# Kernel tuning notes

Hardware: AMD Instinct MI355X
Metric: run time of the kernel (lower is better)

The kernel has to match this reference:

```python
import jax, jax.numpy as jnp
import numpy as np
import math

N, S, C, K, V = 32, 4096, 1, 512, 128
TARGET_SCALE = 0.06  # normalize_scale == embedding_scale when normalize=True


def setup_inputs() -> dict:
    key = jax.random.key(0)
    k1, k2 = jax.random.split(key)
    x0 = jax.random.normal(k1, (N, S, C, V), dtype=jnp.float32)
    emb = jax.random.normal(k2, (C, K, V), dtype=jnp.float32) * TARGET_SCALE
    # after_update(): renormalize each code vector to norm = embedding_scale*sqrt(V)
    tn = TARGET_SCALE * math.sqrt(V)
    emb = emb * (tn / jnp.linalg.norm(emb, axis=2, keepdims=True))
    return {"x0": x0, "embedding0": emb}


def _vq_forward(x0, embedding0):
    tn = TARGET_SCALE * math.sqrt(V)
    # normalize inputs and codebook to the same norm (normalize=True path)
    x = tn * x0 / jnp.linalg.norm(x0, axis=3, keepdims=True)              # (N,S,C,V)
    emb = tn * embedding0 / jnp.linalg.norm(embedding0, axis=2, keepdims=True)  # (C,K,V)

    xf = x.reshape(N * S, C, V)
    x2 = jnp.sum(xf * xf, axis=2)                     # (NS, C)
    e2 = jnp.sum(emb * emb, axis=2)                   # (C, K)
    dots = jnp.einsum('ncv,ckv->nck', xf, emb)        # (NS, C, K)
    d2 = x2[:, :, None] + e2[None, :, :] - 2.0 * dots
    index = jnp.argmin(d2, axis=2)                    # (NS, C) int

    # entropy of code usage: histc over n_classes, normalized by len(index)=NS
    hist = jnp.zeros((K,), jnp.float32).at[index.reshape(-1)].add(1.0)
    prob = hist / float(N * S)
    entropy = -jnp.sum(jnp.where(hist > 0, prob * jnp.log(jnp.where(hist > 0, prob, 1.0)), 0.0))

    # gather selected code vectors per channel
    output = emb[jnp.arange(C)[None, :], index]       # (NS, C, V)
    output = output.reshape(x.shape)                  # (N,S,C,V)

    sg = jax.lax.stop_gradient
    out0 = sg(output - x) + x                                              # straight-through
    out1 = jnp.sum((sg(x) - output) ** 2, axis=3)                          # codebook loss (N,S,C)
    out2 = jnp.sum((x - sg(output)) ** 2, axis=3) + jnp.sum((x - x0) ** 2, axis=3)  # commitment + norm penalty
    return out0, out1, out2, entropy


def reference(x0, embedding0):
    return _vq_forward(x0, embedding0)
```

## Files before the change

kernel.cpp:

```cpp
#include <hip/hip_runtime.h>
#include <math.h>

#define VDIM   128
#define KCODES 512
#define NROWS  (32 * 4096)
#define TILE_ROWS 512
#define NBLK (NROWS / TILE_ROWS)
#define TN 0.67882250993908565f

typedef __attribute__((ext_vector_type(8))) short bf16x8;
typedef __attribute__((ext_vector_type(4))) float f32x4;

__device__ __forceinline__ unsigned short f2bf(float f) {
    unsigned u = __float_as_uint(f);
    unsigned r = u + 0x7FFFu + ((u >> 16) & 1u);
    return (unsigned short)(r >> 16);
}

__device__ __forceinline__ bf16x8 pack8(f32x4 a, f32x4 b) {
    bf16x8 v;
    v[0] = (short)f2bf(a[0]); v[1] = (short)f2bf(a[1]);
    v[2] = (short)f2bf(a[2]); v[3] = (short)f2bf(a[3]);
    v[4] = (short)f2bf(b[0]); v[5] = (short)f2bf(b[1]);
    v[6] = (short)f2bf(b[2]); v[7] = (short)f2bf(b[3]);
    return v;
}

__global__ __launch_bounds__(1024, 1) void vq_fused(
        const float* __restrict__ x0,
        const float* __restrict__ emb0,
        unsigned short* __restrict__ hist_part,
        float* __restrict__ out0,
        float* __restrict__ out1,
        float* __restrict__ out2) {
    __shared__ uint4 sB[8192];
    __shared__ float sscale[KCODES];
    __shared__ int   shist[KCODES];

    int t = threadIdx.x;
    int w = t >> 6;
    int l = t & 63;
    int n15 = l & 15;
    int q = l >> 4;

    int rowbase = blockIdx.x * TILE_ROWS + (w << 5);
    f32x4 ax[2][4][2];
    #pragma unroll
    for (int s = 0; s < 2; ++s) {
        const float* xrow = x0 + (size_t)(rowbase + (s << 4) + n15) * VDIM + (q << 3);
        #pragma unroll
        for (int kc = 0; kc < 4; ++kc) {
            const f32x4* xp = (const f32x4*)(xrow + (kc << 5));
            ax[s][kc][0] = xp[0];
            ax[s][kc][1] = xp[1];
        }
    }

    if (t < KCODES) shist[t] = 0;

    #pragma unroll 4
    for (int i = 0; i < 32; ++i) {
        int k = (w << 5) + i;
        const float* row = emb0 + (size_t)k * VDIM;
        float a = row[l];
        float b = row[l + 64];
        float ss = a * a + b * b;
        #pragma unroll
        for (int off = 32; off; off >>= 1) ss += __shfl_xor(ss, off);
        if (l == 0) sscale[k] = TN / sqrtf(ss);
    }
    __syncthreads();

    #pragma unroll
    for (int i = 0; i < 8; ++i) {
        int g = (i << 10) + t;
        int k = ((g >> 8) << 4) | (g & 15);
        int d0 = ((g >> 4) & 15) << 3;
        float s = sscale[k];
        const f32x4* ep = (const f32x4*)(emb0 + (size_t)k * VDIM + d0);
        f32x4 a = ep[0], b = ep[1];
        f32x4 as, bs;
        as[0] = a[0] * s; as[1] = a[1] * s; as[2] = a[2] * s; as[3] = a[3] * s;
        bs[0] = b[0] * s; bs[1] = b[1] * s; bs[2] = b[2] * s; bs[3] = b[3] * s;
        ((bf16x8*)sB)[g] = pack8(as, bs);
    }

    bf16x8 afr[2][4];
    float nsq[2];
    #pragma unroll
    for (int s = 0; s < 2; ++s) {
        float p0 = 0.f, p1 = 0.f;
        #pragma unroll
        for (int kc = 0; kc < 4; ++kc) {
            f32x4 a = ax[s][kc][0], b = ax[s][kc][1];
            p0 = fmaf(a[0], a[0], p0); p1 = fmaf(a[1], a[1], p1);
            p0 = fmaf(a[2], a[2], p0); p1 = fmaf(a[3], a[3], p1);
            p0 = fmaf(b[0], b[0], p0); p1 = fmaf(b[1], b[1], p1);
            p0 = fmaf(b[2], b[2], p0); p1 = fmaf(b[3], b[3], p1);
            afr[s][kc] = pack8(a, b);
        }
        nsq[s] = p0 + p1;
        nsq[s] += __shfl_xor(nsq[s], 16, 64);
        nsq[s] += __shfl_xor(nsq[s], 32, 64);
    }

    float best[2][4];
    int   bidx[2][4];
    #pragma unroll
    for (int s = 0; s < 2; ++s)
        #pragma unroll
        for (int r = 0; r < 4; ++r) { best[s][r] = -3.4e38f; bidx[s][r] = 0; }

    const f32x4 zero4 = {0.f, 0.f, 0.f, 0.f};

    __syncthreads();

    #pragma unroll 2
    for (int cn = 0; cn < 32; ++cn) {
        const bf16x8* bls = ((const bf16x8*)sB) + (cn << 8) + l;
        bf16x8 b0 = bls[0], b1 = bls[64], b2 = bls[128], b3 = bls[192];
        int nbase = (cn << 4) + n15;
        #pragma unroll
        for (int s = 0; s < 2; ++s) {
            f32x4 acc = __builtin_amdgcn_mfma_f32_16x16x32_bf16(afr[s][0], b0, zero4, 0, 0, 0);
            acc = __builtin_amdgcn_mfma_f32_16x16x32_bf16(afr[s][1], b1, acc, 0, 0, 0);
            acc = __builtin_amdgcn_mfma_f32_16x16x32_bf16(afr[s][2], b2, acc, 0, 0, 0);
            acc = __builtin_amdgcn_mfma_f32_16x16x32_bf16(afr[s][3], b3, acc, 0, 0, 0);
            #pragma unroll
            for (int r = 0; r < 4; ++r) {
                float d = acc[r];
                if (d > best[s][r]) { best[s][r] = d; bidx[s][r] = nbase; }
            }
        }
    }

    #pragma unroll
    for (int m = 1; m <= 8; m <<= 1) {
        #pragma unroll
        for (int s = 0; s < 2; ++s)
            #pragma unroll
            for (int r = 0; r < 4; ++r) {
                float ov = __shfl_xor(best[s][r], m, 64);
                int   oi = __shfl_xor(bidx[s][r], m, 64);
                if (ov > best[s][r] || (ov == best[s][r] && oi < bidx[s][r])) {
                    best[s][r] = ov; bidx[s][r] = oi;
                }
            }
    }

    size_t wrow = (size_t)rowbase;
    #pragma unroll
    for (int p = 0; p < 16; ++p) {
        const int a0 = 2 * p, a1 = 2 * p + 1;
        int biLo = __shfl(bidx[a0 >> 4][a0 & 3], ((a0 >> 2) & 3) << 4, 64);
        int biHi = __shfl(bidx[a1 >> 4][a1 & 3], ((a1 >> 2) & 3) << 4, 64);
        int bi = (l >= 32) ? biHi : biLo;
        float s = sscale[bi];
        int v4 = l & 31;
        size_t grow = wrow + (p << 1) + (l >> 5);
        f32x4 e = *((const f32x4*)(emb0 + (size_t)bi * VDIM) + v4);
        f32x4 o;
        o[0] = e[0] * s; o[1] = e[1] * s; o[2] = e[2] * s; o[3] = e[3] * s;
        __builtin_nontemporal_store(o, (f32x4*)(out0 + grow * (size_t)VDIM) + v4);
    }

    #pragma unroll
    for (int s = 0; s < 2; ++s)
        #pragma unroll
        for (int r = 0; r < 4; ++r) {
            int src = (l & 12) << 2;
            float dv = __shfl(best[s][r], src, 64);
            int   bv = __shfl(bidx[s][r], src, 64);
            float nn = __shfl(nsq[s], l & 15, 64);
            bool act = (l < 32) && ((l >> 4) == s) && ((l & 3) == r);
            if (act) {
                size_t row = wrow + l;
                float sc = TN / sqrtf(nn);
                float o1 = 2.f * TN * TN - 2.f * sc * dv;
                __builtin_nontemporal_store(o1, &out1[row]);
                float sm = sc - 1.f;
                __builtin_nontemporal_store(o1 + sm * sm * nn, &out2[row]);
                atomicAdd(&shist[bv], 1);
            }
        }

    __syncthreads();

    if (t < KCODES)
        hist_part[((size_t)blockIdx.x << 9) + t] = (unsigned short)shist[t];
}

__global__ __launch_bounds__(1024) void entropy_k(
        const unsigned short* __restrict__ hp,
        float* __restrict__ out) {
    __shared__ int   s2[1024];
    __shared__ float red[8];
    int t = threadIdx.x;
    int c = t & 511;
    int half = t >> 9;
    int sum = 0;
    #pragma unroll 8
    for (int b = half * 128; b < half * 128 + 128; ++b)
        sum += hp[(b << 9) + c];
    s2[t] = sum;
    __syncthreads();
    if (t < 512) {
        float h = (float)(s2[t] + s2[t + 512]);
        float p = h / (float)NROWS;
        float term = (h > 0.f) ? p * logf(p) : 0.f;
        #pragma unroll
        for (int off = 32; off; off >>= 1) term += __shfl_xor(term, off);
        if ((t & 63) == 0) red[t >> 6] = term;
    }
    __syncthreads();
    if (t == 0) {
        float ssum = 0.f;
        #pragma unroll
        for (int i = 0; i < 8; i++) ssum += red[i];
        out[0] = -ssum;
    }
}

extern "C" void kernel_launch(void* const* d_in, const int* in_sizes, int n_in,
                              void* d_out, int out_size, void* d_ws, size_t ws_size,
                              hipStream_t stream) {
    const float* x0   = (const float*)d_in[0];
    const float* emb0 = (const float*)d_in[1];

    unsigned short* hist_part = (unsigned short*)d_ws;

    float* out  = (float*)d_out;
    float* out0 = out;
    float* out1 = out0 + (size_t)NROWS * VDIM;
    float* out2 = out1 + NROWS;
    float* oent = out2 + NROWS;

    vq_fused<<<NBLK, 1024, 0, stream>>>(x0, emb0, hist_part, out0, out1, out2);
    entropy_k<<<1, 1024, 0, stream>>>(hist_part, oent);
}
```

Baseline: 158.9 us.

## Halve block size, give each wave 64 rows, and stage index via LDS

Blocks drop from 1024 to 512 threads, and each wave now processes 64 rows (four 16-row MFMA groups) instead of 32. This reuses each codebook B-fragment read from LDS across twice as many rows, and launch bounds now allow two blocks per CU. The second half of the x loads is issued after the codebook norm pass so its latency is hidden, with sched_barriers to keep that ordering. The epilogue writes best indices to shared memory and reads them back instead of using shuffle broadcasts. The cost is higher register pressure from 16 accumulator/argmax slots per lane and larger per-block LDS, which could limit occupancy.

```diff
diff --git a/kernel.cpp b/kernel.cpp
--- a/kernel.cpp
+++ b/kernel.cpp
@@ -26,7 +26,7 @@
     return v;
 }
 
-__global__ __launch_bounds__(1024, 1) void vq_fused(
+__global__ __launch_bounds__(512, 2) void vq_fused(
         const float* __restrict__ x0,
         const float* __restrict__ emb0,
         unsigned short* __restrict__ hist_part,
@@ -36,6 +36,7 @@
     __shared__ uint4 sB[8192];
     __shared__ float sscale[KCODES];
     __shared__ int   shist[KCODES];
+    __shared__ int   sbesti[TILE_ROWS];
 
     int t = threadIdx.x;
     int w = t >> 6;
@@ -43,24 +44,26 @@
     int n15 = l & 15;
     int q = l >> 4;
 
-    int rowbase = blockIdx.x * TILE_ROWS + (w << 5);
-    f32x4 ax[2][4][2];
+    int rowbase = blockIdx.x * TILE_ROWS + (w << 6);
+
+    f32x4 ax01[2][4][2];
     #pragma unroll
     for (int s = 0; s < 2; ++s) {
         const float* xrow = x0 + (size_t)(rowbase + (s << 4) + n15) * VDIM + (q << 3);
         #pragma unroll
         for (int kc = 0; kc < 4; ++kc) {
             const f32x4* xp = (const f32x4*)(xrow + (kc << 5));
-            ax[s][kc][0] = xp[0];
-            ax[s][kc][1] = xp[1];
-        }
-    }
+            ax01[s][kc][0] = xp[0];
+            ax01[s][kc][1] = xp[1];
+        }
+    }
+    __builtin_amdgcn_sched_barrier(0);
 
     if (t < KCODES) shist[t] = 0;
 
     #pragma unroll 4
-    for (int i = 0; i < 32; ++i) {
-        int k = (w << 5) + i;
+    for (int i = 0; i < 64; ++i) {
+        int k = (w << 6) + i;
         const float* row = emb0 + (size_t)k * VDIM;
         float a = row[l];
         float b = row[l + 64];
@@ -69,11 +72,25 @@
         for (int off = 32; off; off >>= 1) ss += __shfl_xor(ss, off);
         if (l == 0) sscale[k] = TN / sqrtf(ss);
     }
-    __syncthreads();
-
-    #pragma unroll
-    for (int i = 0; i < 8; ++i) {
-        int g = (i << 10) + t;
+
+    f32x4 ax23[2][4][2];
+    #pragma unroll
+    for (int s = 0; s < 2; ++s) {
+        const float* xrow = x0 + (size_t)(rowbase + ((s + 2) << 4) + n15) * VDIM + (q << 3);
+        #pragma unroll
+        for (int kc = 0; kc < 4; ++kc) {
+            const f32x4* xp = (const f32x4*)(xrow + (kc << 5));
+            ax23[s][kc][0] = xp[0];
+            ax23[s][kc][1] = xp[1];
+        }
+    }
+    __builtin_amdgcn_sched_barrier(0);
+
+    __syncthreads();
+
+    #pragma unroll
+    for (int i = 0; i < 16; ++i) {
+        int g = (i << 9) + t;
         int k = ((g >> 8) << 4) | (g & 15);
         int d0 = ((g >> 4) & 15) << 3;
         float s = sscale[k];
@@ -85,14 +102,14 @@
         ((bf16x8*)sB)[g] = pack8(as, bs);
     }
 
-    bf16x8 afr[2][4];
-    float nsq[2];
+    bf16x8 afr[4][4];
+    float nsq[4];
     #pragma unroll
     for (int s = 0; s < 2; ++s) {
         float p0 = 0.f, p1 = 0.f;
         #pragma unroll
         for (int kc = 0; kc < 4; ++kc) {
-            f32x4 a = ax[s][kc][0], b = ax[s][kc][1];
+            f32x4 a = ax01[s][kc][0], b = ax01[s][kc][1];
             p0 = fmaf(a[0], a[0], p0); p1 = fmaf(a[1], a[1], p1);
             p0 = fmaf(a[2], a[2], p0); p1 = fmaf(a[3], a[3], p1);
             p0 = fmaf(b[0], b[0], p0); p1 = fmaf(b[1], b[1], p1);
@@ -104,16 +121,33 @@
         nsq[s] += __shfl_xor(nsq[s], 32, 64);
     }
 
-    float best[2][4];
-    int   bidx[2][4];
-    #pragma unroll
-    for (int s = 0; s < 2; ++s)
+    __syncthreads();
+
+    #pragma unroll
+    for (int s = 0; s < 2; ++s) {
+        float p0 = 0.f, p1 = 0.f;
+        #pragma unroll
+        for (int kc = 0; kc < 4; ++kc) {
+            f32x4 a = ax23[s][kc][0], b = ax23[s][kc][1];
+            p0 = fmaf(a[0], a[0], p0); p1 = fmaf(a[1], a[1], p1);
+            p0 = fmaf(a[2], a[2], p0); p1 = fmaf(a[3], a[3], p1);
+            p0 = fmaf(b[0], b[0], p0); p1 = fmaf(b[1], b[1], p1);
+            p0 = fmaf(b[2], b[2], p0); p1 = fmaf(b[3], b[3], p1);
+            afr[s + 2][kc] = pack8(a, b);
+        }
+        nsq[s + 2] = p0 + p1;
+        nsq[s + 2] += __shfl_xor(nsq[s + 2], 16, 64);
+        nsq[s + 2] += __shfl_xor(nsq[s + 2], 32, 64);
+    }
+
+    float best[4][4];
+    int   bidx[4][4];
+    #pragma unroll
+    for (int s = 0; s < 4; ++s)
         #pragma unroll
         for (int r = 0; r < 4; ++r) { best[s][r] = -3.4e38f; bidx[s][r] = 0; }
 
     const f32x4 zero4 = {0.f, 0.f, 0.f, 0.f};
-
-    __syncthreads();
 
     #pragma unroll 2
     for (int cn = 0; cn < 32; ++cn) {
@@ -121,7 +155,7 @@
         bf16x8 b0 = bls[0], b1 = bls[64], b2 = bls[128], b3 = bls[192];
         int nbase = (cn << 4) + n15;
         #pragma unroll
-        for (int s = 0; s < 2; ++s) {
+        for (int s = 0; s < 4; ++s) {
             f32x4 acc = __builtin_amdgcn_mfma_f32_16x16x32_bf16(afr[s][0], b0, zero4, 0, 0, 0);
             acc = __builtin_amdgcn_mfma_f32_16x16x32_bf16(afr[s][1], b1, acc, 0, 0, 0);
             acc = __builtin_amdgcn_mfma_f32_16x16x32_bf16(afr[s][2], b2, acc, 0, 0, 0);
@@ -137,7 +171,7 @@
     #pragma unroll
     for (int m = 1; m <= 8; m <<= 1) {
         #pragma unroll
-        for (int s = 0; s < 2; ++s)
+        for (int s = 0; s < 4; ++s)
             #pragma unroll
             for (int r = 0; r < 4; ++r) {
                 float ov = __shfl_xor(best[s][r], m, 64);
@@ -148,41 +182,38 @@
             }
     }
 
-    size_t wrow = (size_t)rowbase;
-    #pragma unroll
-    for (int p = 0; p < 16; ++p) {
-        const int a0 = 2 * p, a1 = 2 * p + 1;
-        int biLo = __shfl(bidx[a0 >> 4][a0 & 3], ((a0 >> 2) & 3) << 4, 64);
-        int biHi = __shfl(bidx[a1 >> 4][a1 & 3], ((a1 >> 2) & 3) << 4, 64);
-        int bi = (l >= 32) ? biHi : biLo;
+    int r3 = l & 3;
+    bool own = (((l & 15) >> 2) == q);
+    if (own) {
+        #pragma unroll
+        for (int s = 0; s < 4; ++s) {
+            int rl = (s << 4) + (l & 15);
+            size_t row = (size_t)rowbase + rl;
+            float dv = best[s][r3];
+            int   bv = bidx[s][r3];
+            float nn = nsq[s];
+            float sc = TN / sqrtf(nn);
+            float o1 = 2.f * TN * TN - 2.f * sc * dv;
+            __builtin_nontemporal_store(o1, &out1[row]);
+            float sm = sc - 1.f;
+            __builtin_nontemporal_store(o1 + sm * sm * nn, &out2[row]);
+            atomicAdd(&shist[bv], 1);
+            sbesti[(w << 6) + rl] = bv;
+        }
+    }
+
+    #pragma unroll 8
+    for (int p = 0; p < 32; ++p) {
+        int rl = (p << 1) + (l >> 5);
+        int bi = sbesti[(w << 6) + rl];
         float s = sscale[bi];
         int v4 = l & 31;
-        size_t grow = wrow + (p << 1) + (l >> 5);
         f32x4 e = *((const f32x4*)(emb0 + (size_t)bi * VDIM) + v4);
         f32x4 o;
         o[0] = e[0] * s; o[1] = e[1] * s; o[2] = e[2] * s; o[3] = e[3] * s;
-        __builtin_nontemporal_store(o, (f32x4*)(out0 + grow * (size_t)VDIM) + v4);
-    }
-
-    #pragma unroll
-    for (int s = 0; s < 2; ++s)
-        #pragma unroll
-        for (int r = 0; r < 4; ++r) {
-            int src = (l & 12) << 2;
-            float dv = __shfl(best[s][r], src, 64);
-            int   bv = __shfl(bidx[s][r], src, 64);
-            float nn = __shfl(nsq[s], l & 15, 64);
-            bool act = (l < 32) && ((l >> 4) == s) && ((l & 3) == r);
-            if (act) {
-                size_t row = wrow + l;
-                float sc = TN / sqrtf(nn);
-                float o1 = 2.f * TN * TN - 2.f * sc * dv;
-                __builtin_nontemporal_store(o1, &out1[row]);
-                float sm = sc - 1.f;
-                __builtin_nontemporal_store(o1 + sm * sm * nn, &out2[row]);
-                atomicAdd(&shist[bv], 1);
-            }
-        }
+        __builtin_nontemporal_store(
+            o, (f32x4*)(out0 + ((size_t)rowbase + rl) * (size_t)VDIM) + v4);
+    }
 
     __syncthreads();
 
@@ -235,6 +266,6 @@
     float* out2 = out1 + NROWS;
     float* oent = out2 + NROWS;
 
-    vq_fused<<<NBLK, 1024, 0, stream>>>(x0, emb0, hist_part, out0, out1, out2);
+    vq_fused<<<NBLK, 512, 0, stream>>>(x0, emb0, hist_part, out0, out1, out2);
     entropy_k<<<1, 1024, 0, stream>>>(hist_part, oent);
 }
```

Result: slower. 188.6 us (+18.7%).
